# Optimization experiments

Measured on AMD Instinct MI355X. Metric: run time of the kernel, lower is better.

Reference implementation:

```python
import jax, jax.numpy as jnp
import numpy as np

EPS = 1e-8

def setup_inputs() -> dict:
    key = jax.random.key(0)
    k1, k2, k3, k4 = jax.random.split(key, 4)
    b, in_c, out_c, style_c, k, h, w = 8, 512, 512, 512, 3, 64, 64
    return {
        "input": jax.random.normal(k1, (b, in_c, h, w), dtype=jnp.float32),
        "style": jax.random.normal(k2, (b, style_c), dtype=jnp.float32),
        "w_affine": jax.random.normal(k3, (in_c, style_c), dtype=jnp.float32),  # Linear weight, init N(0,1), runtime-scaled
        "b_affine": jnp.ones((1, in_c), dtype=jnp.float32),                     # Bias init_value=1.0
        "w_conv": jax.random.normal(k4, (out_c, in_c, k, k), dtype=jnp.float32),
    }

def reference(input, style, w_affine, b_affine, w_conv):
    b, in_c, h, w = input.shape
    out_c, _, kh, kw = w_conv.shape
    # Equalized-LR runtime scales (lr_mul=1):
    affine_scale = 1.0 / (w_affine.shape[1] ** 0.5)          # he_std for Linear
    conv_scale = 1.0 / ((in_c * kh * kw) ** 0.5)             # he_std for conv weight
    # affine: Linear + Bias (bias initialized to 1.0)
    s = style @ w_affine.T * affine_scale + b_affine          # [b, in_c]
    # modulate: per-sample weight tensor [b, out_c, in_c, kh, kw]
    wgt = s[:, None, :, None, None] * (w_conv * conv_scale)[None]
    # demodulate
    demod = jax.lax.rsqrt(jnp.sum(wgt * wgt, axis=(2, 3, 4), keepdims=True) + EPS)
    wgt = wgt * demod
    # grouped conv with groups = batch (stride=1, padding=1)
    x = input.reshape(1, b * in_c, h, w)
    wgt = wgt.reshape(b * out_c, in_c, kh, kw)
    out = jax.lax.conv_general_dilated(
        x, wgt,
        window_strides=(1, 1),
        padding=[(1, 1), (1, 1)],
        dimension_numbers=("NCHW", "OIHW", "NCHW"),
        feature_group_count=b,
    )
    return out.reshape(b, out_c, h, w)
```

## Files before the change

### kernel.cpp

```cpp
#include <hip/hip_runtime.h>
#include <hip/hip_bf16.h>

#define BB 8
#define CIN 512
#define COUT 512
#define HH 64
#define WW 64

#define AFF_SCALE 0.044194173824159216f
#define CONV_SCALE 0.014731391274719736f
#define CONV_SCALE2 (1.0f/4608.0f)

typedef short s16x8 __attribute__((ext_vector_type(8)));
typedef float f32x16 __attribute__((ext_vector_type(16)));

__device__ __forceinline__ unsigned short f2bf(float f) {
  __hip_bfloat16 h = __float2bfloat16(f);
  return *reinterpret_cast<unsigned short*>(&h);
}

__device__ __forceinline__ void gload_lds16(const void* g, void* l) {
  __builtin_amdgcn_global_load_lds(
      (const __attribute__((address_space(1))) unsigned int*)g,
      (__attribute__((address_space(3))) unsigned int*)l, 16, 0, 0);
}

__global__ __launch_bounds__(256) void affine_kernel(
    const float* __restrict__ style, const float* __restrict__ wa,
    const float* __restrict__ ba, float* __restrict__ smod) {
  int wid  = (blockIdx.x << 2) + (threadIdx.x >> 6);
  int lane = threadIdx.x & 63;
  int b  = wid >> 9;
  int ic = wid & 511;
  const float* s = style + b * CIN;
  const float* w = wa + (size_t)ic * CIN;
  float sum = 0.f;
#pragma unroll
  for (int k = 0; k < CIN / 64; ++k) sum += s[lane + 64 * k] * w[lane + 64 * k];
#pragma unroll
  for (int off = 32; off; off >>= 1) sum += __shfl_down(sum, off, 64);
  if (lane == 0) smod[wid] = sum * AFF_SCALE + ba[ic];
}

__global__ __launch_bounds__(256) void wsq_kernel(
    const float* __restrict__ wc, float* __restrict__ wsq) {
  int i = blockIdx.x * 256 + threadIdx.x;
  const float* p = wc + (size_t)i * 9;
  float s = 0.f;
#pragma unroll
  for (int k = 0; k < 9; ++k) { float v = p[k]; s += v * v; }
  wsq[i] = s;
}

__global__ __launch_bounds__(256) void demod_kernel(
    const float* __restrict__ smod, const float* __restrict__ wsq,
    float* __restrict__ demod) {
  int wid  = (blockIdx.x << 2) + (threadIdx.x >> 6);
  int lane = threadIdx.x & 63;
  int b  = wid >> 9;
  int oc = wid & 511;
  const float* s = smod + b * CIN;
  const float* w = wsq + (size_t)oc * CIN;
  float sum = 0.f;
#pragma unroll
  for (int k = 0; k < CIN / 64; ++k) {
    float sv = s[lane + 64 * k];
    sum += sv * sv * w[lane + 64 * k];
  }
#pragma unroll
  for (int off = 32; off; off >>= 1) sum += __shfl_down(sum, off, 64);
  if (lane == 0) demod[wid] = rsqrtf(sum * CONV_SCALE2 + 1e-8f) * CONV_SCALE;
}

__global__ __launch_bounds__(256) void premod_kernel(
    const float* __restrict__ xin, const float* __restrict__ smod,
    ushort* __restrict__ xt) {
  int n = blockIdx.x * 256 + threadIdx.x;
  int kg = n & 3;
  int x  = (n >> 2) & 63;
  int y  = (n >> 8) & 63;
  int g  = (n >> 14) & 15;
  int b  = n >> 18;
  int ic0 = g * 32 + kg * 8;
  const float* sp = smod + b * CIN + ic0;
  const float* xp = xin + (((size_t)b * CIN + ic0) * HH + y) * WW + x;
  s16x8 o;
#pragma unroll
  for (int j = 0; j < 8; ++j) {
    float v = xp[(size_t)j * HH * WW] * sp[j];
    o[j] = (short)f2bf(v);
  }
  *(s16x8*)(xt + (size_t)n * 8) = o;
}

__global__ __launch_bounds__(256) void wpack_kernel(
    const float* __restrict__ wc, ushort* __restrict__ wfrag) {
  int n = blockIdx.x * 256 + threadIdx.x;
  int l    = n & 63;
  int ks   = (n >> 6) & 1;
  int mf   = (n >> 7) & 15;
  int widx = n >> 11;
  int g = widx / 9, tap = widx % 9;
  int kh = tap / 3, kw = tap - kh * 3;
  int oc  = mf * 32 + (l & 31);
  int ic0 = g * 32 + ks * 16 + 8 * (l >> 5);
  s16x8 o;
#pragma unroll
  for (int j = 0; j < 8; ++j) {
    float v = wc[((size_t)oc * CIN + ic0 + j) * 9 + kh * 3 + kw];
    o[j] = (short)f2bf(v);
  }
  *(s16x8*)(wfrag + (size_t)n * 8) = o;
}

#define XS_ROW 4224
#define XS_BUF (4 * XS_ROW)

#define MFMA1(A_, B_, C_) __builtin_amdgcn_mfma_f32_32x32x16_bf16(A_, B_, C_, 0, 0, 0)

#define MH(W_, S_, KF) \
  __builtin_amdgcn_s_setprio(1); \
  acc[0][0] = MFMA1(W_[0], S_[0 + (KF)], acc[0][0]); \
  acc[1][0] = MFMA1(W_[1], S_[0 + (KF)], acc[1][0]); \
  acc[0][1] = MFMA1(W_[0], S_[2 + (KF)], acc[0][1]); \
  acc[1][1] = MFMA1(W_[1], S_[2 + (KF)], acc[1][1]); \
  __builtin_amdgcn_s_setprio(0);

#define WPRE(W_, TP, KS) \
  W_[0] = *(const s16x8*)(wg + (size_t)(TP) * 32768 + (KS) * 1024); \
  W_[1] = *(const s16x8*)(wg + (size_t)(TP) * 32768 + 2048 + (KS) * 1024);

#define LOADSLOT(S, RR, DXI) \
  S[0] = *(const s16x8*)(xs_r + (wr + (RR)) * XS_ROW + addrV[0][DXI][0]); \
  S[1] = *(const s16x8*)(xs_r + (wr + (RR)) * XS_ROW + addrV[0][DXI][1]); \
  S[2] = *(const s16x8*)(xs_r + (wr + (RR)) * XS_ROW + addrV[1][DXI][0]); \
  S[3] = *(const s16x8*)(xs_r + (wr + (RR)) * XS_ROW + addrV[1][DXI][1]);

#define GBARRIER \
  __builtin_amdgcn_sched_barrier(0); \
  asm volatile("s_waitcnt vmcnt(16)" ::: "memory"); \
  __builtin_amdgcn_sched_barrier(0); \
  __builtin_amdgcn_s_barrier(); \
  __builtin_amdgcn_sched_barrier(0);

#define GBODY(GG, TAILC) \
{ \
  const char* xs_r = (const char*)lds + (GG) * XS_BUF; \
  char* xs_w = lds + ((GG) ^ 1) * XS_BUF; \
  const char* wg = wl + (size_t)(g2 * 18 + (GG) * 9) * 32768; \
  LOADSLOT(bA, 0, 0) LOADSLOT(bB, 1, 0) \
   MH(wA, bA, 0) WPRE(wC, 3, 0) LOADSLOT(bC, 2, 0) \
         MH(wB, bA, 1) WPRE(wA, 3, 1) \
   MH(wC, bB, 0) WPRE(wB, 6, 0) LOADSLOT(bA, 0, 1) \
         MH(wA, bB, 1) WPRE(wC, 6, 1) \
   MH(wB, bC, 0) WPRE(wA, 1, 0) LOADSLOT(bB, 1, 1) \
         MH(wC, bC, 1) WPRE(wB, 1, 1) \
   MH(wA, bA, 0) WPRE(wC, 4, 0) LOADSLOT(bC, 2, 1) \
         MH(wB, bA, 1) WPRE(wA, 4, 1) \
   MH(wC, bB, 0) WPRE(wB, 7, 0) LOADSLOT(bA, 0, 2) \
         MH(wA, bB, 1) WPRE(wC, 7, 1) \
   if (TAILC) stage4(xtb, (size_t)(b * 16 + g2 * 2 + (GG) + 1) * 262144, srcoff, xs_w, lds_woff, y0); \
         MH(wB, bC, 0) WPRE(wA, 2, 0) LOADSLOT(bB, 1, 2) \
         MH(wC, bC, 1) WPRE(wB, 2, 1) \
   MH(wA, bA, 0) WPRE(wC, 5, 0) LOADSLOT(bC, 2, 2) \
         MH(wB, bA, 1) WPRE(wA, 5, 1) \
   MH(wC, bB, 0) WPRE(wB, 8, 0) \
         MH(wA, bB, 1) WPRE(wC, 8, 1) \
   MH(wB, bC, 0) WPRE(wA, 9, 0) \
         MH(wC, bC, 1) WPRE(wB, 9, 1) \
  if (TAILC) { GBARRIER } \
}

__device__ __forceinline__ void stage4(const char* xtb, size_t gbase, int srcoff,
                                       char* xs_w, int lds_woff, int y0) {
  __builtin_amdgcn_sched_barrier(0);
#pragma unroll
  for (int r = 0; r < 4; ++r) {
    int gy = y0 - 1 + r;
    if (gy >= 0 && gy < HH)
      gload_lds16(xtb + gbase + (size_t)gy * 4096 + srcoff,
                  xs_w + r * XS_ROW + lds_woff);
  }
  __builtin_amdgcn_sched_barrier(0);
}

__global__ __launch_bounds__(256, 3) void conv_mfma(
    const ushort* __restrict__ xt,
    const ushort* __restrict__ wfrag,
    const float* __restrict__ demod,
    float* __restrict__ out) {
  __shared__ char lds[2 * XS_BUF];

  int tid = threadIdx.x;
  int l = tid & 63, w = tid >> 6;
  int wm = w >> 1, wr = w & 1;
  int bid = blockIdx.x;
  int ocb = bid & 3;
  int b   = (bid >> 2) & 7;
  int yt  = bid >> 5;
  int y0  = yt * 2;

  f32x16 acc[2][2];
#pragma unroll
  for (int i = 0; i < 2; ++i)
#pragma unroll
    for (int j = 0; j < 2; ++j)
#pragma unroll
      for (int e = 0; e < 16; ++e) acc[i][j][e] = 0.f;

  if (tid < 64) {
    int buf = tid & 1, side = (tid >> 1) & 1, kgz = (tid >> 2) & 3, r = (tid >> 4) & 3;
    int chunk = side ? (260 + kgz) : kgz;
    *(int4*)(lds + buf * XS_BUF + r * XS_ROW + chunk * 16) = int4{0, 0, 0, 0};
  }
  if (y0 == 0) {
    for (int i = tid; i < 528; i += 256) {
      int buf = i & 1, chunk = i >> 1;
      *(int4*)(lds + buf * XS_BUF + chunk * 16) = int4{0, 0, 0, 0};
    }
  }
  if (y0 == 62) {
    for (int i = tid; i < 528; i += 256) {
      int buf = i & 1, chunk = i >> 1;
      *(int4*)(lds + buf * XS_BUF + 3 * XS_ROW + chunk * 16) = int4{0, 0, 0, 0};
    }
  }

  int addrV[2][3][2];
  {
    int lm = l & 31, kh2 = l >> 5;
#pragma unroll
    for (int ph = 0; ph < 2; ++ph)
#pragma unroll
      for (int dxi = 0; dxi < 3; ++dxi)
#pragma unroll
        for (int ks = 0; ks < 2; ++ks) {
          int col = ph * 32 + lm + dxi;
          int kg  = kh2 + 2 * ks;
          addrV[ph][dxi][ks] = (col * 4 + (kg ^ ((col >> 1) & 3))) * 16;
        }
  }

  int col_s = 1 + w * 16 + (l >> 2);
  int srcoff = (col_s - 1) * 64 + ((l & 3) ^ ((col_s >> 1) & 3)) * 16;
  int lds_woff = 64 + w * 1024;

  const char* xtb = (const char*)xt;
  const char* wl = (const char*)wfrag + (size_t)(ocb * 4 + wm * 2) * 2048 + (size_t)l * 16;

  s16x8 wA[2], wB[2], wC[2];
  wA[0] = *(const s16x8*)(wl);
  wA[1] = *(const s16x8*)(wl + 2048);
  wB[0] = *(const s16x8*)(wl + 1024);
  wB[1] = *(const s16x8*)(wl + 3072);

  {
    size_t gbase = (size_t)(b * 16) * 262144;
#pragma unroll
    for (int r = 0; r < 4; ++r) {
      int gy = y0 - 1 + r;
      if (gy >= 0 && gy < HH)
        gload_lds16(xtb + gbase + (size_t)gy * 4096 + srcoff,
                    lds + r * XS_ROW + lds_woff);
    }
  }
  __syncthreads();

  s16x8 bA[4], bB[4], bC[4];

  for (int g2 = 0; g2 < 8; ++g2) {
    GBODY(0, true)
    GBODY(1, (g2 < 7))
  }

  int gy = y0 + wr;
  int colbase = l & 31;
  int rowadd = 4 * (l >> 5);
#pragma unroll
  for (int q = 0; q < 2; ++q) {
#pragma unroll
    for (int reg = 0; reg < 16; ++reg) {
      int row = (reg & 3) + 8 * (reg >> 2) + rowadd;
      int oc = ocb * 128 + (wm * 2 + q) * 32 + row;
      float dm = demod[b * COUT + oc];
      size_t obase = ((size_t)(b * COUT + oc)) * 4096 + gy * 64;
      out[obase + colbase]      = acc[q][0][reg] * dm;
      out[obase + 32 + colbase] = acc[q][1][reg] * dm;
    }
  }
}

extern "C" void kernel_launch(void* const* d_in, const int* in_sizes, int n_in,
                              void* d_out, int out_size, void* d_ws, size_t ws_size,
                              hipStream_t stream) {
  const float* input = (const float*)d_in[0];
  const float* style = (const float*)d_in[1];
  const float* wa    = (const float*)d_in[2];
  const float* ba    = (const float*)d_in[3];
  const float* wconv = (const float*)d_in[4];
  float* out = (float*)d_out;

  float* smod  = (float*)d_ws;
  float* demod = smod + BB * CIN;
  float* wsq   = demod + BB * COUT;
  ushort* wfrag = (ushort*)(wsq + (size_t)COUT * CIN);
  ushort* xt    = wfrag + (size_t)16 * 9 * 32 * 64 * 8;

  affine_kernel<<<BB * CIN / 4, 256, 0, stream>>>(style, wa, ba, smod);
  wsq_kernel<<<COUT * CIN / 256, 256, 0, stream>>>(wconv, wsq);
  demod_kernel<<<BB * COUT / 4, 256, 0, stream>>>(smod, wsq, demod);
  wpack_kernel<<<16 * 9 * 32 * 64 / 256, 256, 0, stream>>>(wconv, wfrag);
  premod_kernel<<<BB * 16 * 64 * 64 * 4 / 256, 256, 0, stream>>>(input, smod, xt);
  conv_mfma<<<4 * BB * 32, 256, 0, stream>>>(xt, wfrag, demod, out);
}
```

Baseline: 175.0 us.

## Reorder tap traversal and deepen weight prefetch in MFMA conv pipeline

Reorders the packed weight taps so kh varies fastest, letting the inner loop walk rows within a column. The kernel now keeps two B-fragment buffers instead of three and four weight register sets instead of three, prefetching weights two taps ahead rather than one. The barrier wait count is adjusted for the extra loads in flight, and it now also waits for LDS reads. The aim is to hide global weight-load latency behind MFMAs, at the cost of more vector registers, which could hurt occupancy under launch_bounds(256,3).

```diff
diff --git a/kernel.cpp b/kernel.cpp
--- a/kernel.cpp
+++ b/kernel.cpp
@@ -100,8 +100,8 @@
   int ks   = (n >> 6) & 1;
   int mf   = (n >> 7) & 15;
   int widx = n >> 11;
-  int g = widx / 9, tap = widx % 9;
-  int kh = tap / 3, kw = tap - kh * 3;
+  int g = widx / 9, p = widx % 9;
+  int kh = p % 3, kw = p / 3;
   int oc  = mf * 32 + (l & 31);
   int ic0 = g * 32 + ks * 16 + 8 * (l >> 5);
   s16x8 o;
@@ -118,56 +118,56 @@
 
 #define MFMA1(A_, B_, C_) __builtin_amdgcn_mfma_f32_32x32x16_bf16(A_, B_, C_, 0, 0, 0)
 
-#define MH(W_, S_, KF) \
+#define MH4(W_, S_, KS) \
   __builtin_amdgcn_s_setprio(1); \
-  acc[0][0] = MFMA1(W_[0], S_[0 + (KF)], acc[0][0]); \
-  acc[1][0] = MFMA1(W_[1], S_[0 + (KF)], acc[1][0]); \
-  acc[0][1] = MFMA1(W_[0], S_[2 + (KF)], acc[0][1]); \
-  acc[1][1] = MFMA1(W_[1], S_[2 + (KF)], acc[1][1]); \
+  acc[0][0] = MFMA1(W_[0], S_[0 + (KS)], acc[0][0]); \
+  acc[1][0] = MFMA1(W_[1], S_[0 + (KS)], acc[1][0]); \
+  acc[0][1] = MFMA1(W_[0], S_[2 + (KS)], acc[0][1]); \
+  acc[1][1] = MFMA1(W_[1], S_[2 + (KS)], acc[1][1]); \
   __builtin_amdgcn_s_setprio(0);
 
-#define WPRE(W_, TP, KS) \
-  W_[0] = *(const s16x8*)(wg + (size_t)(TP) * 32768 + (KS) * 1024); \
-  W_[1] = *(const s16x8*)(wg + (size_t)(TP) * 32768 + 2048 + (KS) * 1024);
-
-#define LOADSLOT(S, RR, DXI) \
-  S[0] = *(const s16x8*)(xs_r + (wr + (RR)) * XS_ROW + addrV[0][DXI][0]); \
-  S[1] = *(const s16x8*)(xs_r + (wr + (RR)) * XS_ROW + addrV[0][DXI][1]); \
-  S[2] = *(const s16x8*)(xs_r + (wr + (RR)) * XS_ROW + addrV[1][DXI][0]); \
-  S[3] = *(const s16x8*)(xs_r + (wr + (RR)) * XS_ROW + addrV[1][DXI][1]);
+#define WPRE2(W_, P, KS) \
+  W_[0] = *(const s16x8*)(wg + (size_t)(P) * 32768 + (KS) * 1024); \
+  W_[1] = *(const s16x8*)(wg + (size_t)(P) * 32768 + 2048 + (KS) * 1024);
+
+#define BLOAD(S_, P) \
+  S_[0] = *(const s16x8*)(xs_r + (wr + (P) % 3) * XS_ROW + addrV[0][(P) / 3][0]); \
+  S_[1] = *(const s16x8*)(xs_r + (wr + (P) % 3) * XS_ROW + addrV[0][(P) / 3][1]); \
+  S_[2] = *(const s16x8*)(xs_r + (wr + (P) % 3) * XS_ROW + addrV[1][(P) / 3][0]); \
+  S_[3] = *(const s16x8*)(xs_r + (wr + (P) % 3) * XS_ROW + addrV[1][(P) / 3][1]);
 
 #define GBARRIER \
   __builtin_amdgcn_sched_barrier(0); \
-  asm volatile("s_waitcnt vmcnt(16)" ::: "memory"); \
+  asm volatile("s_waitcnt vmcnt(24) lgkmcnt(0)" ::: "memory"); \
   __builtin_amdgcn_sched_barrier(0); \
   __builtin_amdgcn_s_barrier(); \
   __builtin_amdgcn_sched_barrier(0);
 
-#define GBODY(GG, TAILC) \
+#define GBODY(GG, W0_, W1_, W2_, W3_, TAILC) \
 { \
   const char* xs_r = (const char*)lds + (GG) * XS_BUF; \
   char* xs_w = lds + ((GG) ^ 1) * XS_BUF; \
   const char* wg = wl + (size_t)(g2 * 18 + (GG) * 9) * 32768; \
-  LOADSLOT(bA, 0, 0) LOADSLOT(bB, 1, 0) \
-   MH(wA, bA, 0) WPRE(wC, 3, 0) LOADSLOT(bC, 2, 0) \
-         MH(wB, bA, 1) WPRE(wA, 3, 1) \
-   MH(wC, bB, 0) WPRE(wB, 6, 0) LOADSLOT(bA, 0, 1) \
-         MH(wA, bB, 1) WPRE(wC, 6, 1) \
-   MH(wB, bC, 0) WPRE(wA, 1, 0) LOADSLOT(bB, 1, 1) \
-         MH(wC, bC, 1) WPRE(wB, 1, 1) \
-   MH(wA, bA, 0) WPRE(wC, 4, 0) LOADSLOT(bC, 2, 1) \
-         MH(wB, bA, 1) WPRE(wA, 4, 1) \
-   MH(wC, bB, 0) WPRE(wB, 7, 0) LOADSLOT(bA, 0, 2) \
-         MH(wA, bB, 1) WPRE(wC, 7, 1) \
+  BLOAD(b0, 0) \
+   MH4(W0_, b0, 0) WPRE2(W0_, 2, 0) BLOAD(b1, 1) \
+         MH4(W1_, b0, 1) WPRE2(W1_, 2, 1) \
+   MH4(W2_, b1, 0) WPRE2(W2_, 3, 0) BLOAD(b0, 2) \
+         MH4(W3_, b1, 1) WPRE2(W3_, 3, 1) \
+   MH4(W0_, b0, 0) WPRE2(W0_, 4, 0) BLOAD(b1, 3) \
+         MH4(W1_, b0, 1) WPRE2(W1_, 4, 1) \
    if (TAILC) stage4(xtb, (size_t)(b * 16 + g2 * 2 + (GG) + 1) * 262144, srcoff, xs_w, lds_woff, y0); \
-         MH(wB, bC, 0) WPRE(wA, 2, 0) LOADSLOT(bB, 1, 2) \
-         MH(wC, bC, 1) WPRE(wB, 2, 1) \
-   MH(wA, bA, 0) WPRE(wC, 5, 0) LOADSLOT(bC, 2, 2) \
-         MH(wB, bA, 1) WPRE(wA, 5, 1) \
-   MH(wC, bB, 0) WPRE(wB, 8, 0) \
-         MH(wA, bB, 1) WPRE(wC, 8, 1) \
-   MH(wB, bC, 0) WPRE(wA, 9, 0) \
-         MH(wC, bC, 1) WPRE(wB, 9, 1) \
+         MH4(W2_, b1, 0) WPRE2(W2_, 5, 0) BLOAD(b0, 4) \
+         MH4(W3_, b1, 1) WPRE2(W3_, 5, 1) \
+   MH4(W0_, b0, 0) WPRE2(W0_, 6, 0) BLOAD(b1, 5) \
+         MH4(W1_, b0, 1) WPRE2(W1_, 6, 1) \
+   MH4(W2_, b1, 0) WPRE2(W2_, 7, 0) BLOAD(b0, 6) \
+         MH4(W3_, b1, 1) WPRE2(W3_, 7, 1) \
+   MH4(W0_, b0, 0) WPRE2(W0_, 8, 0) BLOAD(b1, 7) \
+         MH4(W1_, b0, 1) WPRE2(W1_, 8, 1) \
+   MH4(W2_, b1, 0) WPRE2(W2_, 9, 0) BLOAD(b0, 8) \
+         MH4(W3_, b1, 1) WPRE2(W3_, 9, 1) \
+   MH4(W0_, b0, 0) WPRE2(W0_, 10, 0) \
+         MH4(W1_, b0, 1) WPRE2(W1_, 10, 1) \
   if (TAILC) { GBARRIER } \
 }
 
@@ -248,11 +248,15 @@
   const char* xtb = (const char*)xt;
   const char* wl = (const char*)wfrag + (size_t)(ocb * 4 + wm * 2) * 2048 + (size_t)l * 16;
 
-  s16x8 wA[2], wB[2], wC[2];
-  wA[0] = *(const s16x8*)(wl);
-  wA[1] = *(const s16x8*)(wl + 2048);
-  wB[0] = *(const s16x8*)(wl + 1024);
-  wB[1] = *(const s16x8*)(wl + 3072);
+  s16x8 wSA[2], wSB[2], wSC[2], wSD[2];
+  wSA[0] = *(const s16x8*)(wl);
+  wSA[1] = *(const s16x8*)(wl + 2048);
+  wSB[0] = *(const s16x8*)(wl + 1024);
+  wSB[1] = *(const s16x8*)(wl + 3072);
+  wSC[0] = *(const s16x8*)(wl + 32768);
+  wSC[1] = *(const s16x8*)(wl + 32768 + 2048);
+  wSD[0] = *(const s16x8*)(wl + 32768 + 1024);
+  wSD[1] = *(const s16x8*)(wl + 32768 + 3072);
 
   {
     size_t gbase = (size_t)(b * 16) * 262144;
@@ -266,11 +270,11 @@
   }
   __syncthreads();
 
-  s16x8 bA[4], bB[4], bC[4];
+  s16x8 b0[4], b1[4];
 
   for (int g2 = 0; g2 < 8; ++g2) {
-    GBODY(0, true)
-    GBODY(1, (g2 < 7))
+    GBODY(0, wSA, wSB, wSC, wSD, true)
+    GBODY(1, wSC, wSD, wSA, wSB, (g2 < 7))
   }
 
   int gy = y0 + wr;
```

New measurement: 168.6 us. -3.6%, faster.
